# Kernel tuning notes

Hardware: AMD Instinct MI355X
Metric: run time of the kernel (lower is better)

Reference implementation:

```python
import jax, jax.numpy as jnp
import numpy as np

NUM_HEADS = 2
POOL_K = 256
REPEAT = 20


def setup_inputs() -> dict:
    key = jax.random.key(0)
    k1, k2, k3 = jax.random.split(key, 3)
    C = 6144
    d = C // NUM_HEADS                      # 3072
    N = REPEAT * (d // POOL_K)              # 240, required by Pq add
    x = jax.random.normal(k1, (N, C), dtype=jnp.float32)
    w_qkv = jax.random.normal(k2, (3 * C, C), dtype=jnp.float32) * 0.02
    w_proj = jax.random.normal(k3, (C, C), dtype=jnp.float32) * 0.02
    b_proj = jnp.zeros((C,), dtype=jnp.float32)
    return {"x": x, "w_qkv": w_qkv, "w_proj": w_proj, "b_proj": b_proj}


def reference(x, w_qkv, w_proj, b_proj):
    N, C = x.shape
    H = NUM_HEADS
    d = C // H
    scale = d ** -0.5
    # qkv: (N, 3C) -> (N, 3, H, d) -> (3, H, N, d)
    qkv = (x @ w_qkv.T).reshape(N, 3, H, d).transpose(1, 2, 0, 3)
    q, k, v = qkv[0], qkv[1], qkv[2]        # each (H, N, d)
    # MaxPool1d(256) over last dim, then tile x20 along last dim -> (H, N, N)
    Pq = q.reshape(H, N, d // POOL_K, POOL_K).max(axis=-1)
    Pq = jnp.tile(Pq, (1, 1, REPEAT))       # (H, N, N)
    attn = jnp.einsum('hnd,hmd->hnm', q, k) * scale + 0.1 * Pq
    attn = jax.nn.softmax(attn, axis=-1)
    out = jnp.einsum('hnm,hmd->hnd', attn, v)    # (H, N, d)
    out = out.transpose(1, 0, 2).reshape(N, C)
    return out @ w_proj.T + b_proj
```

## Files before the change

kernel.cpp:

```cpp
#include <hip/hip_runtime.h>
#include <hip/hip_bf16.h>

#define NN 240
#define CC 6144
#define DD 3072
#define C3 18432
#define HH 2

typedef __attribute__((ext_vector_type(8))) short bf16x8;
typedef __attribute__((ext_vector_type(4))) float f32x4;
typedef unsigned short ushort_t;

static __device__ __forceinline__ unsigned short f2bf(float f) {
    __hip_bfloat16 h = __float2bfloat16(f);
    return __builtin_bit_cast(unsigned short, h);
}

#define GLDS16(g, l) __builtin_amdgcn_global_load_lds( \
    (const __attribute__((address_space(1))) void*)(g), \
    (__attribute__((address_space(3))) void*)(l), 16, 0, 0)

__global__ __launch_bounds__(512, 4)
void gemm_p2(const ushort_t* __restrict__ Ab, int lda, long long sAz,
             const float* __restrict__ B, int ldb, long long sBz,
             const float* __restrict__ bias,
             float* __restrict__ C0, long long sC0z,
             float* __restrict__ CP, long long sCPz,
             int ldc, int N, int Kc, int KS,
             ushort_t* __restrict__ Qb) {
    __shared__ ushort_t sA[2][256 * 64];
    __shared__ ushort_t sB[2][64 * 64];

    const int zc = blockIdx.z;
    const int z = zc / KS, kc = zc % KS;
    const ushort_t* Abase = Ab + (size_t)z * sAz + (size_t)kc * Kc;
    const float*    Bbase = B  + (size_t)z * sBz + (size_t)kc * Kc;
    float* Cw = (kc == 0) ? (C0 + (size_t)z * sC0z)
                          : (CP + (size_t)(z * (KS - 1) + kc - 1) * sCPz);

    const int n0 = blockIdx.x * 64;
    const int tid = threadIdx.x, lane = tid & 63, wid = tid >> 6;
    const int wm = wid >> 1, wn = wid & 1;
    const int l16 = lane & 15, lk = lane >> 4;

    const int arow = wid * 32 + (lane >> 3);
    const ushort_t* ap = Abase + (size_t)arow * lda
                         + ((lane & 7) ^ ((lane >> 3) & 7)) * 8;

    const int brow = tid >> 3, boct = tid & 7;
    const float* bp = Bbase + (size_t)(n0 + brow) * ldb + boct * 8;
    const int bws = brow * 64 + ((boct ^ (brow & 7)) * 8);

    const int nt = Kc / 64;
    f32x4 acc[4][2] = {};

    auto ISSUE_A = [&](int t) {
        const ushort_t* a = ap + (size_t)t * 64;
#pragma unroll
        for (int i = 0; i < 4; ++i)
            GLDS16(a + (size_t)i * 8 * lda, &sA[t & 1][(wid * 4 + i) * 512]);
    };
    auto LOAD_B = [&](int t, float4& g0, float4& g1) {
        const float* p = bp + (size_t)t * 64;
        g0 = *(const float4*)p;
        g1 = *(const float4*)(p + 4);
    };
    auto WRITE_B = [&](int t, float4& g0, float4& g1) {
        bf16x8 r;
        r[0] = (short)f2bf(g0.x); r[1] = (short)f2bf(g0.y);
        r[2] = (short)f2bf(g0.z); r[3] = (short)f2bf(g0.w);
        r[4] = (short)f2bf(g1.x); r[5] = (short)f2bf(g1.y);
        r[6] = (short)f2bf(g1.z); r[7] = (short)f2bf(g1.w);
        *(bf16x8*)&sB[t & 1][bws] = r;
    };
    auto MFMA_PH = [&](int t) {
        const char* As = (const char*)sA[t & 1];
        const char* Bs = (const char*)sB[t & 1];
#pragma unroll
        for (int ks = 0; ks < 2; ++ks) {
            bf16x8 af[4], bf[2];
#pragma unroll
            for (int mt = 0; mt < 4; ++mt) {
                int row = wm * 64 + mt * 16 + l16;
                int boff = row * 128 + (((ks * 4 + lk) * 16) ^ ((row & 7) << 4));
                af[mt] = *(const bf16x8*)(As + boff);
            }
#pragma unroll
            for (int nf = 0; nf < 2; ++nf) {
                int row = wn * 32 + nf * 16 + l16;
                int boff = row * 128 + (((ks * 4 + lk) * 16) ^ ((row & 7) << 4));
                bf[nf] = *(const bf16x8*)(Bs + boff);
            }
            __builtin_amdgcn_s_setprio(1);
#pragma unroll
            for (int mt = 0; mt < 4; ++mt)
#pragma unroll
                for (int nf = 0; nf < 2; ++nf)
                    acc[mt][nf] = __builtin_amdgcn_mfma_f32_16x16x32_bf16(
                        af[mt], bf[nf], acc[mt][nf], 0, 0, 0);
            __builtin_amdgcn_s_setprio(0);
        }
    };

    float4 e0, e1, o0, o1;

    ISSUE_A(0);
    LOAD_B(0, e0, e1);
    if (nt > 1) {
        LOAD_B(1, o0, o1);
        asm volatile("s_waitcnt vmcnt(2)" ::: "memory");
    } else {
        asm volatile("s_waitcnt vmcnt(0)" ::: "memory");
    }
    __builtin_amdgcn_sched_barrier(0);
    WRITE_B(0, e0, e1);
    asm volatile("s_waitcnt lgkmcnt(0)" ::: "memory");
    __builtin_amdgcn_s_barrier();

    auto STEP = [&](int t, float4& w0, float4& w1, float4& r0, float4& r1) {
        const bool ia = (t + 1 < nt);
        const bool ib = (t + 2 < nt);
        if (ia) ISSUE_A(t + 1);
        if (ib) LOAD_B(t + 2, w0, w1);
        __builtin_amdgcn_sched_barrier(0);
        MFMA_PH(t);
        __builtin_amdgcn_sched_barrier(0);
        if (ib) asm volatile("s_waitcnt vmcnt(2)" ::: "memory");
        else    asm volatile("s_waitcnt vmcnt(0)" ::: "memory");
        __builtin_amdgcn_sched_barrier(0);
        if (ia) WRITE_B(t + 1, r0, r1);
        asm volatile("s_waitcnt lgkmcnt(0)" ::: "memory");
        __builtin_amdgcn_s_barrier();
    };

    for (int t = 0; t < nt; t += 2) {
        STEP(t,     e0, e1, o0, o1);
        STEP(t + 1, o0, o1, e0, e1);
    }

#pragma unroll
    for (int mt = 0; mt < 4; ++mt) {
#pragma unroll
        for (int j = 0; j < 4; ++j) {
            int grow = wm * 64 + mt * 16 + lk * 4 + j;
            if (grow < NN) {
#pragma unroll
                for (int nf = 0; nf < 2; ++nf) {
                    int gcol = n0 + wn * 32 + nf * 16 + l16;
                    if (gcol < N) {
                        float v = acc[mt][nf][j];
                        if (kc == 0 && bias) v += bias[gcol];
                        Cw[(size_t)grow * ldc + gcol] = v;
                        if (Qb && gcol < CC)
                            Qb[(size_t)grow * CC + gcol] = f2bf(v);
                    }
                }
            }
        }
    }
}

__global__ __launch_bounds__(256)
void convert_kernel(const float* __restrict__ x, ushort_t* __restrict__ xb) {
    int id = blockIdx.x * 256 + threadIdx.x;
    int row = id / 768, c8 = id % 768;
    bf16x8 o = {};
    if (row < NN) {
        const float* p = x + (size_t)row * CC + c8 * 8;
        float4 a = *(const float4*)p, b = *(const float4*)(p + 4);
        o[0] = (short)f2bf(a.x); o[1] = (short)f2bf(a.y);
        o[2] = (short)f2bf(a.z); o[3] = (short)f2bf(a.w);
        o[4] = (short)f2bf(b.x); o[5] = (short)f2bf(b.y);
        o[6] = (short)f2bf(b.z); o[7] = (short)f2bf(b.w);
    }
    *(bf16x8*)(xb + (size_t)row * CC + c8 * 8) = o;
}

__global__ __launch_bounds__(256)
void reduce_proj(float4* __restrict__ o4, const float4* __restrict__ p4,
                 long long s4) {
    int i = blockIdx.x * 256 + threadIdx.x;
    float4 a = o4[i];
#pragma unroll
    for (int k = 0; k < 2; ++k) {
        float4 b = p4[(size_t)k * s4 + i];
        a.x += b.x; a.y += b.y; a.z += b.z; a.w += b.w;
    }
    o4[i] = a;
}

__global__ __launch_bounds__(256)
void qmax_kernel(const float* __restrict__ qkv, float* __restrict__ qmax) {
    int idx = blockIdx.x * 4 + (threadIdx.x >> 6);
    int lane = threadIdx.x & 63;
    int c = idx % 12;
    int r = idx / 12;
    int n = r % NN, h = r / NN;
    const float* p = qkv + (size_t)n * C3 + h * DD + c * 256 + lane * 4;
    float4 f = *(const float4*)p;
    float m = fmaxf(fmaxf(f.x, f.y), fmaxf(f.z, f.w));
#pragma unroll
    for (int off = 32; off >= 1; off >>= 1)
        m = fmaxf(m, __shfl_xor(m, off));
    if (lane == 0) qmax[idx] = m;
}

__global__ __launch_bounds__(256)
void softmax_kernel(float* __restrict__ attn, const float* __restrict__ gpart,
                    int ksm1, const float* __restrict__ qmax) {
    int r = blockIdx.x * 4 + (threadIdx.x >> 6);
    int lane = threadIdx.x & 63;
    int z = r / NN, n = r % NN;
    float* row = attn + (size_t)r * NN;
    const float* qm = qmax + r * 12;
    const float scale = 0.0180421959f;
    float v[4];
    float mx = -1e30f;
#pragma unroll
    for (int i = 0; i < 4; ++i) {
        int m = lane + 64 * i;
        v[i] = -1e30f;
        if (m < NN) {
            float s = row[m];
            for (int kc = 0; kc < ksm1; ++kc)
                s += gpart[(size_t)(z * ksm1 + kc) * (NN * NN)
                           + (size_t)n * NN + m];
            v[i] = s * scale + 0.1f * qm[m % 12];
        }
        mx = fmaxf(mx, v[i]);
    }
#pragma unroll
    for (int off = 32; off >= 1; off >>= 1)
        mx = fmaxf(mx, __shfl_xor(mx, off));
    float s = 0.f;
#pragma unroll
    for (int i = 0; i < 4; ++i) {
        v[i] = __expf(v[i] - mx);
        s += v[i];
    }
#pragma unroll
    for (int off = 32; off >= 1; off >>= 1)
        s += __shfl_xor(s, off);
    float inv = 1.0f / s;
#pragma unroll
    for (int i = 0; i < 4; ++i) {
        int m = lane + 64 * i;
        if (m < NN) row[m] = v[i] * inv;
    }
}

__global__ __launch_bounds__(256)
void pv_kernel(const float* __restrict__ attn, const float* __restrict__ qkv,
               ushort_t* __restrict__ preb) {
    const int h = blockIdx.z;
    const int n0 = blockIdx.y * 16;
    const int dd0 = blockIdx.x * 256;
    __shared__ float s_attn[16 * NN];
    for (int i = threadIdx.x; i < 16 * NN; i += 256)
        s_attn[i] = attn[(size_t)h * NN * NN + (n0 + i / NN) * NN + (i % NN)];
    __syncthreads();

    const float* vp = qkv + 2 * CC + h * DD + dd0 + threadIdx.x;
    float acc[16] = {};
    for (int m = 0; m < NN; m += 4) {
        float v0 = vp[(size_t)(m + 0) * C3];
        float v1 = vp[(size_t)(m + 1) * C3];
        float v2 = vp[(size_t)(m + 2) * C3];
        float v3 = vp[(size_t)(m + 3) * C3];
#pragma unroll
        for (int i = 0; i < 16; ++i) {
            float4 a = *(const float4*)&s_attn[i * NN + m];
            acc[i] += a.x * v0 + a.y * v1 + a.z * v2 + a.w * v3;
        }
    }
#pragma unroll
    for (int i = 0; i < 16; ++i)
        preb[(size_t)(n0 + i) * CC + h * DD + dd0 + threadIdx.x] =
            f2bf(acc[i]);
}

extern "C" void kernel_launch(void* const* d_in, const int* in_sizes, int n_in,
                              void* d_out, int out_size, void* d_ws, size_t ws_size,
                              hipStream_t stream) {
    const float* x      = (const float*)d_in[0];
    const float* w_qkv  = (const float*)d_in[1];
    const float* w_proj = (const float*)d_in[2];
    const float* b_proj = (const float*)d_in[3];
    float* out = (float*)d_out;

    const size_t f_qkv  = (size_t)NN * C3;
    const size_t f_attn = (size_t)HH * NN * NN;
    const size_t f_qmax = (size_t)HH * NN * 12;
    float* qkv   = (float*)d_ws;
    float* attn  = qkv + f_qkv;
    float* qmaxb = attn + f_attn;
    ushort_t* xb   = (ushort_t*)(qmaxb + f_qmax);
    ushort_t* qb   = xb + (size_t)256 * CC;
    ushort_t* preb = qb + (size_t)256 * CC;
    float* gpart = (float*)(preb + (size_t)256 * CC);

    convert_kernel<<<768, 256, 0, stream>>>(x, xb);

    gemm_p2<<<dim3(C3 / 64, 1, 1), 512, 0, stream>>>(
        xb, CC, 0LL, w_qkv, CC, 0LL, nullptr,
        qkv, 0LL, gpart, 0LL,
        C3, C3, CC, 1, qb);

    qmax_kernel<<<1440, 256, 0, stream>>>(qkv, qmaxb);

    gemm_p2<<<dim3(4, 1, HH * 24), 512, 0, stream>>>(
        qb, CC, (long long)DD,
        qkv + CC, C3, (long long)DD, nullptr,
        attn, (long long)(NN * NN), gpart, (long long)(NN * NN),
        NN, NN, DD / 24, 24, nullptr);

    softmax_kernel<<<120, 256, 0, stream>>>(attn, gpart, 23, qmaxb);

    pv_kernel<<<dim3(12, 15, HH), 256, 0, stream>>>(attn, qkv, preb);

    gemm_p2<<<dim3(CC / 64, 1, 3), 512, 0, stream>>>(
        preb, CC, 0LL, w_proj, CC, 0LL, b_proj,
        out, 0LL, gpart, (long long)((size_t)NN * CC),
        CC, CC, CC / 3, 3, nullptr);
    reduce_proj<<<1440, 256, 0, stream>>>((float4*)out, (const float4*)gpart,
        (long long)((size_t)NN * CC / 4));
}
```

Baseline: 341.6 us.

## Halve GEMM N-tile to 32 columns and rework the load pipeline waits

The GEMM tile width in N drops from 64 to 32 columns, which doubles the grid for the QKV, QK^T and projection GEMMs. The aim is better spread across the many compute units on a weight-bandwidth-bound problem with only 240 rows. The B-load path now uses one float4 per thread with row clamping, and the pipeline is restructured to issue unconditionally (clamped tile indices) with fixed vmcnt waits. Each A tile is now reused across fewer columns, so total A (activation) traffic from L2 doubles, and MFMA work per LDS read is lower.

```diff
diff --git a/kernel.cpp b/kernel.cpp
--- a/kernel.cpp
+++ b/kernel.cpp
@@ -21,7 +21,7 @@
     (__attribute__((address_space(3))) void*)(l), 16, 0, 0)
 
 __global__ __launch_bounds__(512, 4)
-void gemm_p2(const ushort_t* __restrict__ Ab, int lda, long long sAz,
+void gemm_v6(const ushort_t* __restrict__ Ab, int lda, long long sAz,
              const float* __restrict__ B, int ldb, long long sBz,
              const float* __restrict__ bias,
              float* __restrict__ C0, long long sC0z,
@@ -29,7 +29,7 @@
              int ldc, int N, int Kc, int KS,
              ushort_t* __restrict__ Qb) {
     __shared__ ushort_t sA[2][256 * 64];
-    __shared__ ushort_t sB[2][64 * 64];
+    __shared__ ushort_t sB[2][32 * 64];
 
     const int zc = blockIdx.z;
     const int z = zc / KS, kc = zc % KS;
@@ -38,7 +38,7 @@
     float* Cw = (kc == 0) ? (C0 + (size_t)z * sC0z)
                           : (CP + (size_t)(z * (KS - 1) + kc - 1) * sCPz);
 
-    const int n0 = blockIdx.x * 64;
+    const int n0 = blockIdx.x * 32;
     const int tid = threadIdx.x, lane = tid & 63, wid = tid >> 6;
     const int wm = wid >> 1, wn = wid & 1;
     const int l16 = lane & 15, lk = lane >> 4;
@@ -47,95 +47,85 @@
     const ushort_t* ap = Abase + (size_t)arow * lda
                          + ((lane & 7) ^ ((lane >> 3) & 7)) * 8;
 
-    const int brow = tid >> 3, boct = tid & 7;
-    const float* bp = Bbase + (size_t)(n0 + brow) * ldb + boct * 8;
-    const int bws = brow * 64 + ((boct ^ (brow & 7)) * 8);
+    const int brow = tid >> 4, bq = tid & 15;
+    int brow_c = n0 + brow; if (brow_c > N - 1) brow_c = N - 1;
+    const float* bp = Bbase + (size_t)brow_c * ldb + bq * 4;
+    const int bws = brow * 128 + ((((bq >> 1) ^ (brow & 7)) << 4) + (bq & 1) * 8);
 
     const int nt = Kc / 64;
-    f32x4 acc[4][2] = {};
-
-    auto ISSUE_A = [&](int t) {
+    f32x4 acc[4] = {};
+
+    auto ISSUE_A = [&](int t, int par) {
         const ushort_t* a = ap + (size_t)t * 64;
 #pragma unroll
         for (int i = 0; i < 4; ++i)
-            GLDS16(a + (size_t)i * 8 * lda, &sA[t & 1][(wid * 4 + i) * 512]);
-    };
-    auto LOAD_B = [&](int t, float4& g0, float4& g1) {
-        const float* p = bp + (size_t)t * 64;
-        g0 = *(const float4*)p;
-        g1 = *(const float4*)(p + 4);
-    };
-    auto WRITE_B = [&](int t, float4& g0, float4& g1) {
-        bf16x8 r;
-        r[0] = (short)f2bf(g0.x); r[1] = (short)f2bf(g0.y);
-        r[2] = (short)f2bf(g0.z); r[3] = (short)f2bf(g0.w);
-        r[4] = (short)f2bf(g1.x); r[5] = (short)f2bf(g1.y);
-        r[6] = (short)f2bf(g1.z); r[7] = (short)f2bf(g1.w);
-        *(bf16x8*)&sB[t & 1][bws] = r;
-    };
-    auto MFMA_PH = [&](int t) {
-        const char* As = (const char*)sA[t & 1];
-        const char* Bs = (const char*)sB[t & 1];
+            GLDS16(a + (size_t)i * 8 * lda, &sA[par][(wid * 4 + i) * 512]);
+    };
+    auto LOAD_B = [&](int t) {
+        return *(const float4*)(bp + (size_t)t * 64);
+    };
+    auto WRITE_B = [&](int par, float4 g) {
+        ushort4 u;
+        u.x = f2bf(g.x); u.y = f2bf(g.y); u.z = f2bf(g.z); u.w = f2bf(g.w);
+        *(ushort4*)(reinterpret_cast<char*>(&sB[par][0]) + bws) = u;
+    };
+    auto MFMA_PH = [&](int cur) {
+        const char* As = (const char*)sA[cur];
+        const char* Bs = (const char*)sB[cur];
 #pragma unroll
         for (int ks = 0; ks < 2; ++ks) {
-            bf16x8 af[4], bf[2];
+            bf16x8 af[4], bf1;
 #pragma unroll
             for (int mt = 0; mt < 4; ++mt) {
                 int row = wm * 64 + mt * 16 + l16;
                 int boff = row * 128 + (((ks * 4 + lk) * 16) ^ ((row & 7) << 4));
                 af[mt] = *(const bf16x8*)(As + boff);
             }
-#pragma unroll
-            for (int nf = 0; nf < 2; ++nf) {
-                int row = wn * 32 + nf * 16 + l16;
+            {
+                int row = wn * 16 + l16;
                 int boff = row * 128 + (((ks * 4 + lk) * 16) ^ ((row & 7) << 4));
-                bf[nf] = *(const bf16x8*)(Bs + boff);
+                bf1 = *(const bf16x8*)(Bs + boff);
             }
             __builtin_amdgcn_s_setprio(1);
 #pragma unroll
             for (int mt = 0; mt < 4; ++mt)
-#pragma unroll
-                for (int nf = 0; nf < 2; ++nf)
-                    acc[mt][nf] = __builtin_amdgcn_mfma_f32_16x16x32_bf16(
-                        af[mt], bf[nf], acc[mt][nf], 0, 0, 0);
+                acc[mt] = __builtin_amdgcn_mfma_f32_16x16x32_bf16(
+                    af[mt], bf1, acc[mt], 0, 0, 0);
             __builtin_amdgcn_s_setprio(0);
         }
     };
 
-    float4 e0, e1, o0, o1;
-
-    ISSUE_A(0);
-    LOAD_B(0, e0, e1);
-    if (nt > 1) {
-        LOAD_B(1, o0, o1);
-        asm volatile("s_waitcnt vmcnt(2)" ::: "memory");
-    } else {
-        asm volatile("s_waitcnt vmcnt(0)" ::: "memory");
-    }
+    float4 e, o;
+
+    ISSUE_A(0, 0);
+    e = LOAD_B(0);
+    o = (nt > 1) ? LOAD_B(1) : e;
+    asm volatile("s_waitcnt vmcnt(1)" ::: "memory");
     __builtin_amdgcn_sched_barrier(0);
-    WRITE_B(0, e0, e1);
+    WRITE_B(0, e);
     asm volatile("s_waitcnt lgkmcnt(0)" ::: "memory");
     __builtin_amdgcn_s_barrier();
 
-    auto STEP = [&](int t, float4& w0, float4& w1, float4& r0, float4& r1) {
-        const bool ia = (t + 1 < nt);
-        const bool ib = (t + 2 < nt);
-        if (ia) ISSUE_A(t + 1);
-        if (ib) LOAD_B(t + 2, w0, w1);
+    auto STEP = [&](int t, float4& w, float4& r) {
+        int ta = t + 1 < nt ? t + 1 : nt - 1;
+        int tb = t + 2 < nt ? t + 2 : nt - 1;
+        ISSUE_A(ta, (t + 1) & 1);
+        w = LOAD_B(tb);
         __builtin_amdgcn_sched_barrier(0);
-        MFMA_PH(t);
+        asm volatile("s_waitcnt vmcnt(6)" ::: "memory");
         __builtin_amdgcn_sched_barrier(0);
-        if (ib) asm volatile("s_waitcnt vmcnt(2)" ::: "memory");
-        else    asm volatile("s_waitcnt vmcnt(0)" ::: "memory");
+        MFMA_PH(t & 1);
         __builtin_amdgcn_sched_barrier(0);
-        if (ia) WRITE_B(t + 1, r0, r1);
+        asm volatile("s_waitcnt vmcnt(5)" ::: "memory");
+        __builtin_amdgcn_sched_barrier(0);
+        WRITE_B((t + 1) & 1, r);
         asm volatile("s_waitcnt lgkmcnt(0)" ::: "memory");
         __builtin_amdgcn_s_barrier();
     };
 
     for (int t = 0; t < nt; t += 2) {
-        STEP(t,     e0, e1, o0, o1);
-        STEP(t + 1, o0, o1, e0, e1);
+        STEP(t,     e, o);
+        STEP(t + 1, o, e);
     }
 
 #pragma unroll
@@ -144,16 +134,13 @@
         for (int j = 0; j < 4; ++j) {
             int grow = wm * 64 + mt * 16 + lk * 4 + j;
             if (grow < NN) {
-#pragma unroll
-                for (int nf = 0; nf < 2; ++nf) {
-                    int gcol = n0 + wn * 32 + nf * 16 + l16;
-                    if (gcol < N) {
-                        float v = acc[mt][nf][j];
-                        if (kc == 0 && bias) v += bias[gcol];
-                        Cw[(size_t)grow * ldc + gcol] = v;
-                        if (Qb && gcol < CC)
-                            Qb[(size_t)grow * CC + gcol] = f2bf(v);
-                    }
+                int gcol = n0 + wn * 16 + l16;
+                if (gcol < N) {
+                    float v = acc[mt][j];
+                    if (kc == 0 && bias) v += bias[gcol];
+                    Cw[(size_t)grow * ldc + gcol] = v;
+                    if (Qb && gcol < CC)
+                        Qb[(size_t)grow * CC + gcol] = f2bf(v);
                 }
             }
         }
@@ -301,14 +288,14 @@
 
     convert_kernel<<<768, 256, 0, stream>>>(x, xb);
 
-    gemm_p2<<<dim3(C3 / 64, 1, 1), 512, 0, stream>>>(
+    gemm_v6<<<dim3(C3 / 32, 1, 1), 512, 0, stream>>>(
         xb, CC, 0LL, w_qkv, CC, 0LL, nullptr,
         qkv, 0LL, gpart, 0LL,
         C3, C3, CC, 1, qb);
 
     qmax_kernel<<<1440, 256, 0, stream>>>(qkv, qmaxb);
 
-    gemm_p2<<<dim3(4, 1, HH * 24), 512, 0, stream>>>(
+    gemm_v6<<<dim3(8, 1, HH * 24), 512, 0, stream>>>(
         qb, CC, (long long)DD,
         qkv + CC, C3, (long long)DD, nullptr,
         attn, (long long)(NN * NN), gpart, (long long)(NN * NN),
@@ -318,7 +305,7 @@
 
     pv_kernel<<<dim3(12, 15, HH), 256, 0, stream>>>(attn, qkv, preb);
 
-    gemm_p2<<<dim3(CC / 64, 1, 3), 512, 0, stream>>>(
+    gemm_v6<<<dim3(CC / 32, 1, 3), 512, 0, stream>>>(
         preb, CC, 0LL, w_proj, CC, 0LL, b_proj,
         out, 0LL, gpart, (long long)((size_t)NN * CC),
         CC, CC, CC / 3, 3, nullptr);
```

Measured after the change: 424.9 us. 24.4% more time.

## Stream fp32 B tiles directly to LDS with triple-buffered async pipeline

Applied to the files above, without the earlier changes.

Replaces the register-staged B loads (global fp32 → regs → bf16 convert → LDS write) with direct global-to-LDS async loads of raw fp32 into a triple-buffered LDS area. The bf16 conversion moves to the LDS read side inside the MFMA phase. Prefetch depth grows to two A tiles and three B tiles. The goal is to hide memory latency better and free registers. In exchange it uses more LDS, which lowers occupancy (launch bounds go from 4 to 2), and it repeats the conversion work in every wave that reads the same B data.

```diff
diff --git a/kernel.cpp b/kernel.cpp
--- a/kernel.cpp
+++ b/kernel.cpp
@@ -20,8 +20,8 @@
     (const __attribute__((address_space(1))) void*)(g), \
     (__attribute__((address_space(3))) void*)(l), 16, 0, 0)
 
-__global__ __launch_bounds__(512, 4)
-void gemm_p2(const ushort_t* __restrict__ Ab, int lda, long long sAz,
+__global__ __launch_bounds__(512, 2)
+void gemm_cs(const ushort_t* __restrict__ Ab, int lda, long long sAz,
              const float* __restrict__ B, int ldb, long long sBz,
              const float* __restrict__ bias,
              float* __restrict__ C0, long long sC0z,
@@ -29,7 +29,7 @@
              int ldc, int N, int Kc, int KS,
              ushort_t* __restrict__ Qb) {
     __shared__ ushort_t sA[2][256 * 64];
-    __shared__ ushort_t sB[2][64 * 64];
+    __shared__ float    sB[3][64 * 64];
 
     const int zc = blockIdx.z;
     const int z = zc / KS, kc = zc % KS;
@@ -43,99 +43,88 @@
     const int wm = wid >> 1, wn = wid & 1;
     const int l16 = lane & 15, lk = lane >> 4;
 
-    const int arow = wid * 32 + (lane >> 3);
-    const ushort_t* ap = Abase + (size_t)arow * lda
+    const ushort_t* ap = Abase + (size_t)(wid * 32 + (lane >> 3)) * lda
                          + ((lane & 7) ^ ((lane >> 3) & 7)) * 8;
 
-    const int brow = tid >> 3, boct = tid & 7;
-    const float* bp = Bbase + (size_t)(n0 + brow) * ldb + boct * 8;
-    const int bws = brow * 64 + ((boct ^ (brow & 7)) * 8);
+    long long bofs[2];
+#pragma unroll
+    for (int i = 0; i < 2; ++i) {
+        int cl = wid * 8 + i * 4 + (lane >> 4);
+        int cg = n0 + cl; if (cg > N - 1) cg = N - 1;
+        bofs[i] = (long long)cg * ldb + ((lane & 15) ^ (cl & 7)) * 4;
+    }
 
     const int nt = Kc / 64;
     f32x4 acc[4][2] = {};
 
-    auto ISSUE_A = [&](int t) {
+    auto ISSUE_A = [&](int t, int par) {
         const ushort_t* a = ap + (size_t)t * 64;
+        ushort_t* d = &sA[par][wid * 4 * 512];
 #pragma unroll
         for (int i = 0; i < 4; ++i)
-            GLDS16(a + (size_t)i * 8 * lda, &sA[t & 1][(wid * 4 + i) * 512]);
+            GLDS16(a + (size_t)i * 8 * lda, d + i * 512);
     };
-    auto LOAD_B = [&](int t, float4& g0, float4& g1) {
-        const float* p = bp + (size_t)t * 64;
-        g0 = *(const float4*)p;
-        g1 = *(const float4*)(p + 4);
+    auto ISSUE_B = [&](int t, int par) {
+#pragma unroll
+        for (int i = 0; i < 2; ++i)
+            GLDS16(Bbase + bofs[i] + (size_t)t * 64,
+                   &sB[par][(wid * 8 + i * 4) * 64]);
     };
-    auto WRITE_B = [&](int t, float4& g0, float4& g1) {
-        bf16x8 r;
-        r[0] = (short)f2bf(g0.x); r[1] = (short)f2bf(g0.y);
-        r[2] = (short)f2bf(g0.z); r[3] = (short)f2bf(g0.w);
-        r[4] = (short)f2bf(g1.x); r[5] = (short)f2bf(g1.y);
-        r[6] = (short)f2bf(g1.z); r[7] = (short)f2bf(g1.w);
-        *(bf16x8*)&sB[t & 1][bws] = r;
+    auto PHASE = [&](int ab, int bb, int ks) {
+        const char* As = (const char*)sA[ab];
+        bf16x8 af[4], bfr[2];
+#pragma unroll
+        for (int mt = 0; mt < 4; ++mt) {
+            int row = wm * 64 + mt * 16 + l16;
+            af[mt] = *(const bf16x8*)(As + row * 128
+                        + (((ks * 4 + lk) * 16) ^ ((row & 7) << 4)));
+        }
+#pragma unroll
+        for (int nf = 0; nf < 2; ++nf) {
+            int cl = wn * 32 + nf * 16 + l16;
+            int j2 = 2 * (ks * 4 + lk);
+            const char* cb = (const char*)(&sB[bb][cl * 64]);
+            f32x4 lo = *(const f32x4*)(cb + ((j2 ^ (cl & 7)) * 16));
+            f32x4 hi = *(const f32x4*)(cb + (((j2 + 1) ^ (cl & 7)) * 16));
+            bf16x8 r;
+            r[0] = (short)f2bf(lo[0]); r[1] = (short)f2bf(lo[1]);
+            r[2] = (short)f2bf(lo[2]); r[3] = (short)f2bf(lo[3]);
+            r[4] = (short)f2bf(hi[0]); r[5] = (short)f2bf(hi[1]);
+            r[6] = (short)f2bf(hi[2]); r[7] = (short)f2bf(hi[3]);
+            bfr[nf] = r;
+        }
+        __builtin_amdgcn_s_setprio(1);
+#pragma unroll
+        for (int mt = 0; mt < 4; ++mt)
+#pragma unroll
+            for (int nf = 0; nf < 2; ++nf)
+                acc[mt][nf] = __builtin_amdgcn_mfma_f32_16x16x32_bf16(
+                    af[mt], bfr[nf], acc[mt][nf], 0, 0, 0);
+        __builtin_amdgcn_s_setprio(0);
     };
-    auto MFMA_PH = [&](int t) {
-        const char* As = (const char*)sA[t & 1];
-        const char* Bs = (const char*)sB[t & 1];
-#pragma unroll
-        for (int ks = 0; ks < 2; ++ks) {
-            bf16x8 af[4], bf[2];
-#pragma unroll
-            for (int mt = 0; mt < 4; ++mt) {
-                int row = wm * 64 + mt * 16 + l16;
-                int boff = row * 128 + (((ks * 4 + lk) * 16) ^ ((row & 7) << 4));
-                af[mt] = *(const bf16x8*)(As + boff);
-            }
-#pragma unroll
-            for (int nf = 0; nf < 2; ++nf) {
-                int row = wn * 32 + nf * 16 + l16;
-                int boff = row * 128 + (((ks * 4 + lk) * 16) ^ ((row & 7) << 4));
-                bf[nf] = *(const bf16x8*)(Bs + boff);
-            }
-            __builtin_amdgcn_s_setprio(1);
-#pragma unroll
-            for (int mt = 0; mt < 4; ++mt)
-#pragma unroll
-                for (int nf = 0; nf < 2; ++nf)
-                    acc[mt][nf] = __builtin_amdgcn_mfma_f32_16x16x32_bf16(
-                        af[mt], bf[nf], acc[mt][nf], 0, 0, 0);
-            __builtin_amdgcn_s_setprio(0);
-        }
-    };
-
-    float4 e0, e1, o0, o1;
-
-    ISSUE_A(0);
-    LOAD_B(0, e0, e1);
-    if (nt > 1) {
-        LOAD_B(1, o0, o1);
-        asm volatile("s_waitcnt vmcnt(2)" ::: "memory");
-    } else {
-        asm volatile("s_waitcnt vmcnt(0)" ::: "memory");
-    }
+
+    ISSUE_A(0, 0);
+    ISSUE_B(0, 0);
+    ISSUE_A(nt > 1 ? 1 : 0, 1);
+    ISSUE_B(nt > 1 ? 1 : 0, 1);
+    ISSUE_B(nt > 2 ? 2 : nt - 1, 2 % 3);
+    asm volatile("s_waitcnt vmcnt(8)" ::: "memory");
     __builtin_amdgcn_sched_barrier(0);
-    WRITE_B(0, e0, e1);
-    asm volatile("s_waitcnt lgkmcnt(0)" ::: "memory");
     __builtin_amdgcn_s_barrier();
 
-    auto STEP = [&](int t, float4& w0, float4& w1, float4& r0, float4& r1) {
-        const bool ia = (t + 1 < nt);
-        const bool ib = (t + 2 < nt);
-        if (ia) ISSUE_A(t + 1);
-        if (ib) LOAD_B(t + 2, w0, w1);
+    for (int t = 0; t < nt; ++t) {
+        PHASE(t & 1, t % 3, 0);
+        PHASE(t & 1, t % 3, 1);
+        __builtin_amdgcn_s_barrier();
         __builtin_amdgcn_sched_barrier(0);
-        MFMA_PH(t);
+        int ta = t + 2 < nt ? t + 2 : nt - 1;
+        int tb = t + 3 < nt ? t + 3 : nt - 1;
+        ISSUE_A(ta, t & 1);
+        ISSUE_B(tb, t % 3);
         __builtin_amdgcn_sched_barrier(0);
-        if (ib) asm volatile("s_waitcnt vmcnt(2)" ::: "memory");
-        else    asm volatile("s_waitcnt vmcnt(0)" ::: "memory");
+        asm volatile("s_waitcnt vmcnt(8)" ::: "memory");
         __builtin_amdgcn_sched_barrier(0);
-        if (ia) WRITE_B(t + 1, r0, r1);
-        asm volatile("s_waitcnt lgkmcnt(0)" ::: "memory");
         __builtin_amdgcn_s_barrier();
-    };
-
-    for (int t = 0; t < nt; t += 2) {
-        STEP(t,     e0, e1, o0, o1);
-        STEP(t + 1, o0, o1, e0, e1);
     }
 
 #pragma unroll
@@ -301,14 +290,14 @@
 
     convert_kernel<<<768, 256, 0, stream>>>(x, xb);
 
-    gemm_p2<<<dim3(C3 / 64, 1, 1), 512, 0, stream>>>(
+    gemm_cs<<<dim3(C3 / 64, 1, 1), 512, 0, stream>>>(
         xb, CC, 0LL, w_qkv, CC, 0LL, nullptr,
         qkv, 0LL, gpart, 0LL,
         C3, C3, CC, 1, qb);
 
     qmax_kernel<<<1440, 256, 0, stream>>>(qkv, qmaxb);
 
-    gemm_p2<<<dim3(4, 1, HH * 24), 512, 0, stream>>>(
+    gemm_cs<<<dim3(4, 1, HH * 24), 512, 0, stream>>>(
         qb, CC, (long long)DD,
         qkv + CC, C3, (long long)DD, nullptr,
         attn, (long long)(NN * NN), gpart, (long long)(NN * NN),
@@ -318,7 +307,7 @@
 
     pv_kernel<<<dim3(12, 15, HH), 256, 0, stream>>>(attn, qkv, preb);
 
-    gemm_p2<<<dim3(CC / 64, 1, 3), 512, 0, stream>>>(
+    gemm_cs<<<dim3(CC / 64, 1, 3), 512, 0, stream>>>(
         preb, CC, 0LL, w_proj, CC, 0LL, b_proj,
         out, 0LL, gpart, (long long)((size_t)NN * CC),
         CC, CC, CC / 3, 3, nullptr);
```

Measured after the change: 469.6 us. 1.37x slower.
